# Performance work log

Measured on AMD Instinct MI355X. Metric: run time of the kernel, lower is better.

The kernel has to match this reference:

```python
import jax, jax.numpy as jnp
import numpy as np

R, K, H_IN, W_IN = 512, 17, 56, 56   # rois, keypoints, heatmap size
ROI_H = ROI_W = 96                   # = ceil(BOX_LEN), fixed by construction
BOX_LEN = 95.5                       # all boxes have this side length
A = -0.75                            # PyTorch bicubic coefficient


def _cubic(x):
    x = jnp.abs(x)
    near = ((A + 2.0) * x - (A + 3.0)) * x * x + 1.0
    far = A * (((x - 5.0) * x + 8.0) * x - 4.0)
    return jnp.where(x <= 1.0, near, jnp.where(x < 2.0, far, 0.0))


def _resize_matrix(out_size, in_size):
    """Dense [out,in] bicubic interpolation matrix (align_corners=False, border-replicate)."""
    scale = in_size / out_size
    src = (jnp.arange(out_size, dtype=jnp.float32) + 0.5) * scale - 0.5
    base = jnp.floor(src).astype(jnp.int32)
    taps = base[:, None] + jnp.arange(-1, 3)                      # [out, 4]
    w = _cubic(src[:, None] - taps.astype(jnp.float32))           # weights from unclamped dist
    taps = jnp.clip(taps, 0, in_size - 1)                         # replicate border
    rows = jnp.broadcast_to(jnp.arange(out_size)[:, None], taps.shape)
    return jnp.zeros((out_size, in_size), jnp.float32).at[rows, taps].add(w)


def setup_inputs() -> dict:
    key = jax.random.key(0)
    k1, k2 = jax.random.split(key)
    masks = jax.random.normal(k1, (R, K, H_IN, W_IN), dtype=jnp.float32)
    offs = jax.random.uniform(k2, (R, 2), jnp.float32, 0.0, 400.0)
    # corner format (c0_start, c1_start, c0_end, c1_end); all lengths == BOX_LEN
    boxes = jnp.concatenate([offs, offs + BOX_LEN], axis=1)
    return {"masks": masks, "boxes": boxes}


def reference(masks, boxes):
    My = _resize_matrix(ROI_H, H_IN)   # [ROI_H, H_IN]
    Mx = _resize_matrix(ROI_W, W_IN)   # [ROI_W, W_IN]
    # separable bicubic resize of every ROI heatmap: [R,K,ROI_H,ROI_W]
    roi = jnp.einsum('hi,rkij,wj->rkhw', My, masks, Mx)
    flat = roi.reshape(R, K, ROI_H * ROI_W)
    pos = jnp.argmax(flat, axis=-1)                                # [R,K]
    y = pos // ROI_W
    x = pos % ROI_W
    scores = jnp.take_along_axis(flat, pos[..., None], axis=-1)[..., 0]  # logit at argmax
    len0 = jnp.maximum(boxes[:, 2] - boxes[:, 0], 1.0)
    len1 = jnp.maximum(boxes[:, 3] - boxes[:, 1], 1.0)
    corr0 = (len0 / ROI_H)[:, None]
    corr1 = (len1 / ROI_W)[:, None]
    p0 = (y.astype(jnp.float32) + 0.5) * corr0 + boxes[:, 0:1]
    p1 = (x.astype(jnp.float32) + 0.5) * corr1 + boxes[:, 1:2]
    predictions = jnp.stack([p0, p1, jnp.ones_like(p0)], axis=1)   # [R, n_dim+1, K]
    return predictions, scores
```

## Files before the change

### kernel.cpp

```cpp
#include <hip/hip_runtime.h>

#define R_   512
#define K_   17
#define HIN  56
#define WIN  56
#define OUTS 96
#define NMAP (R_ * K_)
#define NT   96
#define TST  97

struct Tab {
    float w[OUTS][4];
    int   s[OUTS];
    constexpr Tab() : w{}, s{} {
        for (int o = 0; o < OUTS; ++o) {
            float src = ((float)o + 0.5f) * (56.0f / 96.0f) - 0.5f;
            int base = (int)src;
            if ((float)base > src) --base;
            int st = base - 1;
            if (st < 0) st = 0;
            if (st > HIN - 4) st = HIN - 4;
            s[o] = st;
            for (int q = 0; q < 4; ++q) {
                int tap = base - 1 + q;
                float x = src - (float)tap;
                if (x < 0.0f) x = -x;
                const float A = -0.75f;
                float wt;
                if (x <= 1.0f)     wt = ((A + 2.0f) * x - (A + 3.0f)) * x * x + 1.0f;
                else if (x < 2.0f) wt = A * (((x - 5.0f) * x + 8.0f) * x - 4.0f);
                else               wt = 0.0f;
                int p = tap;
                if (p < 0) p = 0;
                if (p > HIN - 1) p = HIN - 1;
                w[o][p - st] += wt;
            }
        }
    }
};
constexpr Tab TAB;

__global__ __launch_bounds__(NT)
void _Keypointer_kernel(const float* __restrict__ masks,
                        const float* __restrict__ boxes,
                        float* __restrict__ out) {
    __shared__ float txm[HIN * TST];
    __shared__ float redv[2];
    __shared__ int   redp[2];

    const int t   = threadIdx.x;
    const int map = blockIdx.x;

    if (t < HIN) {
        float r[WIN];
        const float4* g = (const float4*)(masks + (size_t)map * (HIN * WIN) + t * WIN);
#pragma unroll
        for (int i = 0; i < WIN / 4; ++i) {
            float4 v = g[i];
            r[4 * i + 0] = v.x; r[4 * i + 1] = v.y;
            r[4 * i + 2] = v.z; r[4 * i + 3] = v.w;
        }
        float* dst = txm + t * TST;
#pragma unroll
        for (int o = 0; o < OUTS; ++o) {
            const int   s  = TAB.s[o];
            const float w0 = TAB.w[o][0], w1 = TAB.w[o][1];
            const float w2 = TAB.w[o][2], w3 = TAB.w[o][3];
            dst[o] = fmaf(w3, r[s + 3], fmaf(w2, r[s + 2], fmaf(w1, r[s + 1], w0 * r[s])));
        }
    }
    __syncthreads();

    float c[HIN];
    {
        const float* sp = txm + t;
#pragma unroll
        for (int j = 0; j < HIN; ++j) c[j] = sp[j * TST];
    }
    float best  = -INFINITY;
    int   bestp = 0x7fffffff;
#pragma unroll
    for (int h = 0; h < OUTS; ++h) {
        const int   s  = TAB.s[h];
        const float w0 = TAB.w[h][0], w1 = TAB.w[h][1];
        const float w2 = TAB.w[h][2], w3 = TAB.w[h][3];
        float acc = fmaf(w3, c[s + 3], fmaf(w2, c[s + 2], fmaf(w1, c[s + 1], w0 * c[s])));
        if (acc > best) { best = acc; bestp = h * OUTS + t; }
    }

    if (t < 64) {
        float ov = __shfl_down(best, 32, 64);
        int   op = __shfl_down(bestp, 32, 64);
        if (ov > best || (ov == best && op < bestp)) { best = ov; bestp = op; }
    }
#pragma unroll
    for (int off = 16; off > 0; off >>= 1) {
        float ov = __shfl_down(best, off, 64);
        int   op = __shfl_down(bestp, off, 64);
        if (ov > best || (ov == best && op < bestp)) { best = ov; bestp = op; }
    }
    if ((t & 63) == 0) { redv[t >> 6] = best; redp[t >> 6] = bestp; }
    __syncthreads();

    if (t == 0) {
        if (redv[1] > best || (redv[1] == best && redp[1] < bestp)) {
            best = redv[1]; bestp = redp[1];
        }
        const int r = map / K_, k = map - r * K_;
        const int y = bestp / OUTS, x = bestp - y * OUTS;

        const float b0 = boxes[r * 4 + 0], b1 = boxes[r * 4 + 1];
        const float b2 = boxes[r * 4 + 2], b3 = boxes[r * 4 + 3];
        const float corr0 = fmaxf(b2 - b0, 1.0f) / (float)OUTS;
        const float corr1 = fmaxf(b3 - b1, 1.0f) / (float)OUTS;
        const float p0 = ((float)y + 0.5f) * corr0 + b0;
        const float p1 = ((float)x + 0.5f) * corr1 + b1;

        out[(r * 3 + 0) * K_ + k] = p0;
        out[(r * 3 + 1) * K_ + k] = p1;
        out[(r * 3 + 2) * K_ + k] = 1.0f;
        out[R_ * 3 * K_ + r * K_ + k] = best;
    }
}

extern "C" void kernel_launch(void* const* d_in, const int* in_sizes, int n_in,
                              void* d_out, int out_size, void* d_ws, size_t ws_size,
                              hipStream_t stream) {
    const float* masks = (const float*)d_in[0];
    const float* boxes = (const float*)d_in[1];
    float* out = (float*)d_out;
    _Keypointer_kernel<<<NMAP, NT, 0, stream>>>(masks, boxes, out);
}
```

Measured before the change: 168.7 us.

## Process two maps per block with split-phase row tiles and packed column pass

Each block of 192 threads now handles two heatmaps. The horizontal pass splits each row across three groups of 32 outputs, so more threads participate and registers per thread drop. The map is then processed in two halves of rows through a smaller shared tile with replicated border rows. The vertical pass uses the periodic 12-phase structure of the y weights and packed 2-wide FMAs, giving each thread two columns and 24 rows per phase. The aim is higher occupancy and less idle work in the load phase, at the cost of extra syncs and a more complex argmax reduction whose tie-breaking must still match the reference.

Result: faster. 161.2 us (-4.5%).

```diff
diff --git a/kernel.cpp b/kernel.cpp
--- a/kernel.cpp
+++ b/kernel.cpp
@@ -1,18 +1,29 @@
 #include <hip/hip_runtime.h>
 
-#define R_   512
-#define K_   17
-#define HIN  56
-#define WIN  56
-#define OUTS 96
-#define NMAP (R_ * K_)
-#define NT   96
-#define TST  97
-
-struct Tab {
+#define R_    512
+#define K_    17
+#define HIN   56
+#define WIN   56
+#define OUTS  96
+#define NMAP  (R_ * K_)
+#define NT    192
+#define TS    98
+#define TROWS 32
+
+typedef float v2f __attribute__((ext_vector_type(2)));
+
+constexpr float cubic_c(float xin) {
+    float x = xin < 0.0f ? -xin : xin;
+    const float A = -0.75f;
+    if (x <= 1.0f) return ((A + 2.0f) * x - (A + 3.0f)) * x * x + 1.0f;
+    if (x < 2.0f)  return A * (((x - 5.0f) * x + 8.0f) * x - 4.0f);
+    return 0.0f;
+}
+
+struct XTabT {
     float w[OUTS][4];
     int   s[OUTS];
-    constexpr Tab() : w{}, s{} {
+    constexpr XTabT() : w{}, s{} {
         for (int o = 0; o < OUTS; ++o) {
             float src = ((float)o + 0.5f) * (56.0f / 96.0f) - 0.5f;
             int base = (int)src;
@@ -23,103 +34,178 @@
             s[o] = st;
             for (int q = 0; q < 4; ++q) {
                 int tap = base - 1 + q;
-                float x = src - (float)tap;
-                if (x < 0.0f) x = -x;
-                const float A = -0.75f;
-                float wt;
-                if (x <= 1.0f)     wt = ((A + 2.0f) * x - (A + 3.0f)) * x * x + 1.0f;
-                else if (x < 2.0f) wt = A * (((x - 5.0f) * x + 8.0f) * x - 4.0f);
-                else               wt = 0.0f;
-                int p = tap;
-                if (p < 0) p = 0;
-                if (p > HIN - 1) p = HIN - 1;
+                float wt = cubic_c(src - (float)tap);
+                int p = tap < 0 ? 0 : (tap > HIN - 1 ? HIN - 1 : tap);
                 w[o][p - st] += wt;
             }
         }
     }
 };
-constexpr Tab TAB;
+constexpr XTabT XT;
+
+struct YTabT {
+    float w[12][4];
+    int   d[12];
+    constexpr YTabT() : w{}, d{} {
+        for (int ph = 0; ph < 12; ++ph) {
+            float src = ((float)ph + 0.5f) * (56.0f / 96.0f) - 0.5f;
+            int base = (int)src;
+            if ((float)base > src) --base;
+            d[ph] = base - 1;
+            for (int q = 0; q < 4; ++q)
+                w[ph][q] = cubic_c(src - (float)(base - 1 + q));
+        }
+    }
+};
+constexpr YTabT YT;
+
+template<int G>
+__device__ __forceinline__ void p1_row(const float* __restrict__ gsrc, float out[32]) {
+    constexpr int FS = (G == 0) ? 0 : (G == 1) ? 4 : 9;
+    constexpr int NF = (G == 1) ? 6 : 5;
+    float r[NF * 4];
+    const float4* g4 = (const float4*)gsrc + FS;
+#pragma unroll
+    for (int i = 0; i < NF; ++i) {
+        float4 v = g4[i];
+        r[4*i+0] = v.x; r[4*i+1] = v.y; r[4*i+2] = v.z; r[4*i+3] = v.w;
+    }
+#pragma unroll
+    for (int oo = 0; oo < 32; ++oo) {
+        const int o  = 32 * G + oo;
+        const int rs = XT.s[o] - 4 * FS;
+        out[oo] = fmaf(XT.w[o][3], r[rs+3], fmaf(XT.w[o][2], r[rs+2],
+                  fmaf(XT.w[o][1], r[rs+1], XT.w[o][0] * r[rs])));
+    }
+}
+
+__device__ __forceinline__ void p1_phase(const float* __restrict__ masks, float* tbase,
+                                         int t, int bm0, int j0, bool lowhalf) {
+    const int g = t >> 6;
+    const int w = t & 63;
+    if (w >= 60) return;
+    const int mi = w / 30;
+    const int jr = w - 30 * mi;
+    const int j  = j0 + jr;
+    const float* gsrc = masks + (size_t)(bm0 + mi) * (HIN * WIN) + j * WIN;
+    float out[32];
+    if      (g == 0) p1_row<0>(gsrc, out);
+    else if (g == 1) p1_row<1>(gsrc, out);
+    else             p1_row<2>(gsrc, out);
+    const int phys = lowhalf ? jr + 2 : jr;
+    float* dst = tbase + mi * (TROWS * TS) + phys * TS + 32 * g;
+#pragma unroll
+    for (int i = 0; i < 16; ++i) ((v2f*)dst)[i] = (v2f){out[2*i], out[2*i+1]};
+    if (lowhalf && jr == 0) {
+        float* d0 = tbase + mi * (TROWS * TS) + 32 * g;
+#pragma unroll
+        for (int i = 0; i < 16; ++i) {
+            v2f v = (v2f){out[2*i], out[2*i+1]};
+            ((v2f*)d0)[i] = v;
+            ((v2f*)(d0 + TS))[i] = v;
+        }
+    }
+    if (!lowhalf && jr == 29) {
+        float* d0 = tbase + mi * (TROWS * TS) + 30 * TS + 32 * g;
+#pragma unroll
+        for (int i = 0; i < 16; ++i) {
+            v2f v = (v2f){out[2*i], out[2*i+1]};
+            ((v2f*)d0)[i] = v;
+            ((v2f*)(d0 + TS))[i] = v;
+        }
+    }
+}
+
+__device__ __forceinline__ void p2_block(const float* __restrict__ base, int h0,
+                                         float& bx, int& hx, float& by, int& hy) {
+    v2f c[18];
+#pragma unroll
+    for (int i = 0; i < 18; ++i) c[i] = *(const v2f*)(base + i * TS);
+#pragma unroll
+    for (int hh = 0; hh < 24; ++hh) {
+        const int ph = hh % 12;
+        const int b  = hh / 12;
+        const int i0 = 7 * b + YT.d[ph] + 2;
+        const v2f w0 = {YT.w[ph][0], YT.w[ph][0]};
+        const v2f w1 = {YT.w[ph][1], YT.w[ph][1]};
+        const v2f w2 = {YT.w[ph][2], YT.w[ph][2]};
+        const v2f w3 = {YT.w[ph][3], YT.w[ph][3]};
+        v2f acc = c[i0] * w0;
+        acc = __builtin_elementwise_fma(w1, c[i0+1], acc);
+        acc = __builtin_elementwise_fma(w2, c[i0+2], acc);
+        acc = __builtin_elementwise_fma(w3, c[i0+3], acc);
+        const int h = h0 + hh;
+        bool gx = acc.x > bx; bx = gx ? acc.x : bx; hx = gx ? h : hx;
+        bool gy = acc.y > by; by = gy ? acc.y : by; hy = gy ? h : hy;
+    }
+}
 
 __global__ __launch_bounds__(NT)
 void _Keypointer_kernel(const float* __restrict__ masks,
                         const float* __restrict__ boxes,
                         float* __restrict__ out) {
-    __shared__ float txm[HIN * TST];
-    __shared__ float redv[2];
-    __shared__ int   redp[2];
+    __shared__ float tmp[2 * TROWS * TS];
+    __shared__ float redv[NT];
+    __shared__ int   redp[NT];
 
     const int t   = threadIdx.x;
-    const int map = blockIdx.x;
-
-    if (t < HIN) {
-        float r[WIN];
-        const float4* g = (const float4*)(masks + (size_t)map * (HIN * WIN) + t * WIN);
-#pragma unroll
-        for (int i = 0; i < WIN / 4; ++i) {
-            float4 v = g[i];
-            r[4 * i + 0] = v.x; r[4 * i + 1] = v.y;
-            r[4 * i + 2] = v.z; r[4 * i + 3] = v.w;
-        }
-        float* dst = txm + t * TST;
-#pragma unroll
-        for (int o = 0; o < OUTS; ++o) {
-            const int   s  = TAB.s[o];
-            const float w0 = TAB.w[o][0], w1 = TAB.w[o][1];
-            const float w2 = TAB.w[o][2], w3 = TAB.w[o][3];
-            dst[o] = fmaf(w3, r[s + 3], fmaf(w2, r[s + 2], fmaf(w1, r[s + 1], w0 * r[s])));
-        }
-    }
-    __syncthreads();
-
-    float c[HIN];
-    {
-        const float* sp = txm + t;
-#pragma unroll
-        for (int j = 0; j < HIN; ++j) c[j] = sp[j * TST];
-    }
-    float best  = -INFINITY;
-    int   bestp = 0x7fffffff;
-#pragma unroll
-    for (int h = 0; h < OUTS; ++h) {
-        const int   s  = TAB.s[h];
-        const float w0 = TAB.w[h][0], w1 = TAB.w[h][1];
-        const float w2 = TAB.w[h][2], w3 = TAB.w[h][3];
-        float acc = fmaf(w3, c[s + 3], fmaf(w2, c[s + 2], fmaf(w1, c[s + 1], w0 * c[s])));
-        if (acc > best) { best = acc; bestp = h * OUTS + t; }
-    }
+    const int bm0 = 2 * blockIdx.x;
+
+    p1_phase(masks, tmp, t, bm0, 0, true);
+    __syncthreads();
+
+    const int mi = t / 96;
+    const int v  = t - 96 * mi;
+    const int qq = v / 48;
+    const int p  = v - 48 * qq;
+    const float* pbase = tmp + mi * (TROWS * TS) + (14 * qq) * TS + 2 * p;
+
+    float bx = -INFINITY, by = -INFINITY;
+    int hx = 0, hy = 0;
+    p2_block(pbase, 24 * qq, bx, hx, by, hy);
+    __syncthreads();
+
+    p1_phase(masks, tmp, t, bm0, 26, false);
+    __syncthreads();
+
+    p2_block(pbase, 48 + 24 * qq, bx, hx, by, hy);
+
+    int fx = hx * OUTS + 2 * p;
+    int fy = hy * OUTS + 2 * p + 1;
+    if (by > bx || (by == bx && fy < fx)) { bx = by; fx = fy; }
+    redv[t] = bx; redp[t] = fx;
+    __syncthreads();
 
     if (t < 64) {
-        float ov = __shfl_down(best, 32, 64);
-        int   op = __shfl_down(bestp, 32, 64);
-        if (ov > best || (ov == best && op < bestp)) { best = ov; bestp = op; }
-    }
-#pragma unroll
-    for (int off = 16; off > 0; off >>= 1) {
-        float ov = __shfl_down(best, off, 64);
-        int   op = __shfl_down(bestp, off, 64);
-        if (ov > best || (ov == best && op < bestp)) { best = ov; bestp = op; }
-    }
-    if ((t & 63) == 0) { redv[t >> 6] = best; redp[t >> 6] = bestp; }
-    __syncthreads();
-
-    if (t == 0) {
-        if (redv[1] > best || (redv[1] == best && redp[1] < bestp)) {
-            best = redv[1]; bestp = redp[1];
-        }
-        const int r = map / K_, k = map - r * K_;
-        const int y = bestp / OUTS, x = bestp - y * OUTS;
-
-        const float b0 = boxes[r * 4 + 0], b1 = boxes[r * 4 + 1];
-        const float b2 = boxes[r * 4 + 2], b3 = boxes[r * 4 + 3];
-        const float corr0 = fmaxf(b2 - b0, 1.0f) / (float)OUTS;
-        const float corr1 = fmaxf(b3 - b1, 1.0f) / (float)OUTS;
-        const float p0 = ((float)y + 0.5f) * corr0 + b0;
-        const float p1 = ((float)x + 0.5f) * corr1 + b1;
-
-        out[(r * 3 + 0) * K_ + k] = p0;
-        out[(r * 3 + 1) * K_ + k] = p1;
-        out[(r * 3 + 2) * K_ + k] = 1.0f;
-        out[R_ * 3 * K_ + r * K_ + k] = best;
+        const int m = t >> 5, i = t & 31;
+        const int b0 = m * 96 + i;
+        float bv = redv[b0]; int bp = redp[b0];
+#pragma unroll
+        for (int o = 32; o < 96; o += 32) {
+            float vv = redv[b0 + o]; int pp = redp[b0 + o];
+            if (vv > bv || (vv == bv && pp < bp)) { bv = vv; bp = pp; }
+        }
+#pragma unroll
+        for (int off = 16; off > 0; off >>= 1) {
+            float vv = __shfl_down(bv, off, 32);
+            int   pp = __shfl_down(bp, off, 32);
+            if (vv > bv || (vv == bv && pp < bp)) { bv = vv; bp = pp; }
+        }
+        if (i == 0) {
+            const int map = bm0 + m;
+            const int r = map / K_, k = map - r * K_;
+            const int y = bp / OUTS, x = bp - y * OUTS;
+            const float b0f = boxes[r * 4 + 0], b1f = boxes[r * 4 + 1];
+            const float b2f = boxes[r * 4 + 2], b3f = boxes[r * 4 + 3];
+            const float corr0 = fmaxf(b2f - b0f, 1.0f) / (float)OUTS;
+            const float corr1 = fmaxf(b3f - b1f, 1.0f) / (float)OUTS;
+            const float p0 = ((float)y + 0.5f) * corr0 + b0f;
+            const float p1 = ((float)x + 0.5f) * corr1 + b1f;
+            out[(r * 3 + 0) * K_ + k] = p0;
+            out[(r * 3 + 1) * K_ + k] = p1;
+            out[(r * 3 + 2) * K_ + k] = 1.0f;
+            out[R_ * 3 * K_ + r * K_ + k] = bv;
+        }
     }
 }
 
@@ -129,5 +215,5 @@
     const float* masks = (const float*)d_in[0];
     const float* boxes = (const float*)d_in[1];
     float* out = (float*)d_out;
-    _Keypointer_kernel<<<NMAP, NT, 0, stream>>>(masks, boxes, out);
-}
+    _Keypointer_kernel<<<NMAP / 2, NT, 0, stream>>>(masks, boxes, out);
+}
```
